# Performance work log

Measured on AMD Instinct MI355X. Metric: run time of the kernel, lower is better.

## Reference

```python
import jax, jax.numpy as jnp
import numpy as np

LN_EPS = 1e-5

def _layernorm(x, g, b):
    mu = jnp.mean(x, axis=-1, keepdims=True)
    var = jnp.mean(jnp.square(x - mu), axis=-1, keepdims=True)
    return (x - mu) * jax.lax.rsqrt(var + LN_EPS) * g + b

def setup_inputs() -> dict:
    key = jax.random.key(0)
    B, T, C = 8, 2048, 1024
    ks = jax.random.split(key, 16)
    s = 1.0 / np.sqrt(C)
    inp = {
        'x':   jax.random.normal(ks[0], (B, T, C), dtype=jnp.float32),
        'Wq':  jax.random.uniform(ks[1], (C, C), jnp.float32, -s, s),
        'bq':  jax.random.uniform(ks[2], (C,), jnp.float32, -s, s),
        'Wk':  jax.random.uniform(ks[3], (C, C), jnp.float32, -s, s),
        'bk':  jax.random.uniform(ks[4], (C,), jnp.float32, -s, s),
        'Wv':  jax.random.uniform(ks[5], (C, C), jnp.float32, -s, s),
        'bv':  jax.random.uniform(ks[6], (C,), jnp.float32, -s, s),
        'g1':  jnp.ones((C,), jnp.float32),
        'be1': jnp.zeros((C,), jnp.float32),
        'W1':  jax.random.uniform(ks[7], (C, C), jnp.float32, -s, s),
        'bf1': jax.random.uniform(ks[8], (C,), jnp.float32, -s, s),
        'W2':  jax.random.uniform(ks[9], (C, C), jnp.float32, -s, s),
        'bf2': jax.random.uniform(ks[10], (C,), jnp.float32, -s, s),
        'g2':  jnp.ones((C,), jnp.float32),
        'be2': jnp.zeros((C,), jnp.float32),
    }
    return inp

def reference(x, Wq, bq, Wk, bk, Wv, bv, g1, be1, W1, bf1, W2, bf2, g2, be2):
    B, T, C = x.shape
    q = x @ Wq + bq
    k = x @ Wk + bk
    v = x @ Wv + bv
    # FFT cross-correlation along time axis
    fq = jnp.fft.rfft(q, axis=1)
    fk = jnp.fft.rfft(k, axis=1)
    corr = jnp.fft.irfft(fq * jnp.conj(fk), n=T, axis=1)  # [B,T,C]
    weights = jax.nn.softmax(corr, axis=1)
    # einsum 'btd,btv->btd': weights * sum over v's channel dim
    attn = weights * jnp.sum(v, axis=-1, keepdims=True)
    x = _layernorm(x + attn, g1, be1)
    h = jax.nn.relu(x @ W1 + bf1) @ W2 + bf2
    x = _layernorm(x + h, g2, be2)
    return x
```

## Files before the change

kernel.cpp:

```cpp
#include <hip/hip_runtime.h>
#include <math.h>

#define B_DIM 8
#define T_DIM 2048
#define C_DIM 1024
#define BT_DIM (B_DIM * T_DIM)
#define FSZ ((size_t)BT_DIM * C_DIM)
#define LN_EPS 1e-5f

typedef __bf16 bf16x8 __attribute__((ext_vector_type(8)));
typedef _Float16 f16x8 __attribute__((ext_vector_type(8)));
typedef float f32x4 __attribute__((ext_vector_type(4)));

__device__ __forceinline__ unsigned short f2bf(float f) {
  __bf16 h = (__bf16)f;
  return __builtin_bit_cast(unsigned short, h);
}
__device__ __forceinline__ unsigned short f2h(float f) {
  _Float16 h = (_Float16)f;
  return __builtin_bit_cast(unsigned short, h);
}

__device__ __forceinline__ void gld16(const void* g, void* l) {
  __builtin_amdgcn_global_load_lds(
      (const __attribute__((address_space(1))) unsigned int*)g,
      (__attribute__((address_space(3))) unsigned int*)l, 16, 0, 0);
}

__device__ __forceinline__ int swz(int a) {
  return a ^ (((a >> 4) ^ (a >> 8)) & 15);
}

__device__ __forceinline__ int enc11(int f) {
  return ((f & 3) << 9) | (((f >> 2) & 3) << 7) | (((f >> 4) & 3) << 5) |
         (((f >> 6) & 3) << 3) | (((f >> 8) & 3) << 1) | ((f >> 10) & 1);
}

__global__ __launch_bounds__(256)
void cvt_split_f16_kernel(const float* __restrict__ x, unsigned short* __restrict__ hi,
                          unsigned short* __restrict__ lo) {
  size_t idx = ((size_t)blockIdx.x * 256 + threadIdx.x) * 4;
  float4 v = *(const float4*)(x + idx);
  float f[4] = {v.x, v.y, v.z, v.w};
  unsigned short hv[4], lv[4];
#pragma unroll
  for (int i = 0; i < 4; i++) {
    _Float16 hb = (_Float16)f[i];
    hv[i] = __builtin_bit_cast(unsigned short, hb);
    lv[i] = f2h(f[i] - (float)hb);
  }
  *(ushort4*)(hi + idx) = make_ushort4(hv[0], hv[1], hv[2], hv[3]);
  *(ushort4*)(lo + idx) = make_ushort4(lv[0], lv[1], lv[2], lv[3]);
}

__global__ __launch_bounds__(256)
void wtrans_f16_kernel(const float* __restrict__ W, unsigned short* __restrict__ Wt,
                       int K, int N) {
  __shared__ float tile[32][33];
  const int tid = threadIdx.x;
  const int tx = tid & 31, ty = tid >> 5;
  const int n0 = blockIdx.x * 32, k0 = blockIdx.y * 32;
#pragma unroll
  for (int i = 0; i < 4; i++) {
    int row = ty + i * 8;
    tile[row][tx] = W[(size_t)(k0 + row) * N + n0 + tx];
  }
  __syncthreads();
#pragma unroll
  for (int i = 0; i < 4; i++) {
    int row = ty + i * 8;
    Wt[(size_t)(n0 + row) * K + k0 + tx] = f2h(tile[tx][row]);
  }
}

__global__ __launch_bounds__(256)
void wtrans_kernel(const float* __restrict__ W, unsigned short* __restrict__ Wt,
                   int K, int N) {
  __shared__ float tile[32][33];
  const int tid = threadIdx.x;
  const int tx = tid & 31, ty = tid >> 5;
  const int n0 = blockIdx.x * 32, k0 = blockIdx.y * 32;
#pragma unroll
  for (int i = 0; i < 4; i++) {
    int row = ty + i * 8;
    tile[row][tx] = W[(size_t)(k0 + row) * N + n0 + tx];
  }
  __syncthreads();
#pragma unroll
  for (int i = 0; i < 4; i++) {
    int row = ty + i * 8;
    Wt[(size_t)(n0 + row) * K + k0 + tx] = f2bf(tile[tx][row]);
  }
}

__global__ __launch_bounds__(256)
void wv_rowsum_kernel(const float* __restrict__ Wv, const float* __restrict__ bv,
                      float* __restrict__ wvsum, float* __restrict__ bvsum) {
  const int r = blockIdx.x;
  const int tid = threadIdx.x;
  const float* src = (r < C_DIM) ? (Wv + (size_t)r * C_DIM) : bv;
  float4 t4 = *(const float4*)(src + (tid << 2));
  float s = t4.x + t4.y + t4.z + t4.w;
#pragma unroll
  for (int off = 32; off > 0; off >>= 1) s += __shfl_down(s, off);
  __shared__ float ps[4];
  if ((tid & 63) == 0) ps[tid >> 6] = s;
  __syncthreads();
  if (tid == 0) {
    float v = ps[0] + ps[1] + ps[2] + ps[3];
    if (r < C_DIM) wvsum[r] = v; else bvsum[0] = v;
  }
}

__global__ __launch_bounds__(256)
void sv_dot_kernel(const float* __restrict__ x, const float* __restrict__ wvsum,
                   const float* __restrict__ bvsum, float* __restrict__ sv) {
  const int r = blockIdx.x;
  const int tid = threadIdx.x;
  float4 a = *(const float4*)(x + (size_t)r * C_DIM + (tid << 2));
  float4 w = *(const float4*)(wvsum + (tid << 2));
  float s = a.x * w.x + a.y * w.y + a.z * w.z + a.w * w.w;
#pragma unroll
  for (int off = 32; off > 0; off >>= 1) s += __shfl_down(s, off);
  __shared__ float ps[4];
  if ((tid & 63) == 0) ps[tid >> 6] = s;
  __syncthreads();
  if (tid == 0) sv[r] = ps[0] + ps[1] + ps[2] + ps[3] + bvsum[0];
}

__global__ __launch_bounds__(256, 2)
void gemm_bf16_kernel(const __bf16* __restrict__ A, const __bf16* __restrict__ Bt,
                      const float* __restrict__ bias, float* Yf, unsigned short* Yb,
                      int K, int N, int do_relu) {
  __shared__ __align__(16) __bf16 As[128 * 32];
  __shared__ __align__(16) __bf16 Bs[128 * 32];
  const int tid = threadIdx.x;
  const int wave = tid >> 6, lane = tid & 63;
  const int wr = wave >> 1, wc = wave & 1;
  const int r15 = lane & 15, kq = lane >> 4;
  const int m0 = blockIdx.y * 128, n0 = blockIdx.x * 128;

  f32x4 acc[4][4] = {};

  for (int k0 = 0; k0 < K; k0 += 32) {
#pragma unroll
    for (int r = 0; r < 2; ++r) {
      int idx = r * 256 + tid;
      int row = idx >> 2;
      int ko = (idx & 3) ^ ((row >> 1) & 3);
      gld16(A + (size_t)(m0 + row) * K + k0 + ko * 8, &As[idx * 8]);
      gld16(Bt + (size_t)(n0 + row) * K + k0 + ko * 8, &Bs[idx * 8]);
    }
    __syncthreads();
    bf16x8 afr[4], bfr[4];
#pragma unroll
    for (int i = 0; i < 4; i++) {
      int ar = wr * 64 + i * 16 + r15;
      afr[i] = *(const bf16x8*)&As[(ar * 4 + (kq ^ ((ar >> 1) & 3))) * 8];
      int br = wc * 64 + i * 16 + r15;
      bfr[i] = *(const bf16x8*)&Bs[(br * 4 + (kq ^ ((br >> 1) & 3))) * 8];
    }
#pragma unroll
    for (int mi = 0; mi < 4; mi++)
#pragma unroll
      for (int ni = 0; ni < 4; ni++)
        acc[mi][ni] = __builtin_amdgcn_mfma_f32_16x16x32_bf16(afr[mi], bfr[ni], acc[mi][ni], 0, 0, 0);
    __syncthreads();
  }

  float bv[4];
#pragma unroll
  for (int ni = 0; ni < 4; ni++) bv[ni] = bias[n0 + wc * 64 + ni * 16 + r15];

#pragma unroll
  for (int mi = 0; mi < 4; mi++)
#pragma unroll
    for (int ni = 0; ni < 4; ni++) {
      const int n = n0 + wc * 64 + ni * 16 + r15;
#pragma unroll
      for (int r = 0; r < 4; r++) {
        const int m = m0 + wr * 64 + mi * 16 + kq * 4 + r;
        float v = acc[mi][ni][r] + bv[ni];
        if (do_relu) v = fmaxf(v, 0.f);
        if (Yf) Yf[(size_t)m * N + n] = v;
        if (Yb) Yb[(size_t)m * N + n] = f2bf(v);
      }
    }
}

__global__ __launch_bounds__(256, 2)
void gemm_qkT_f16_kernel(const _Float16* __restrict__ Ahi, const _Float16* __restrict__ Alo,
                         const _Float16* __restrict__ Bq, const _Float16* __restrict__ Bk,
                         const float* __restrict__ biasq, const float* __restrict__ biask,
                         float* __restrict__ Yq, float* __restrict__ Yk, int K, int N) {
  __shared__ __align__(16) _Float16 Ash[128 * 32];
  __shared__ __align__(16) _Float16 Asl[128 * 32];
  __shared__ __align__(16) _Float16 Bsq[128 * 32];
  __shared__ __align__(16) _Float16 Bsk[128 * 32];
  const int tid = threadIdx.x;
  const int wave = tid >> 6, lane = tid & 63;
  const int wr = wave >> 1, wc = wave & 1;
  const int r15 = lane & 15, kq = lane >> 4;
  const int m0 = blockIdx.y * 128, n0 = blockIdx.x * 128;

  f32x4 accq[4][4] = {};
  f32x4 acck[4][4] = {};

  for (int k0 = 0; k0 < K; k0 += 32) {
#pragma unroll
    for (int r = 0; r < 2; ++r) {
      int idx = r * 256 + tid;
      int row = idx >> 2;
      int ko = (idx & 3) ^ ((row >> 1) & 3);
      size_t ga = (size_t)(m0 + row) * K + k0 + ko * 8;
      size_t gb = (size_t)(n0 + row) * K + k0 + ko * 8;
      gld16(Ahi + ga, &Ash[idx * 8]);
      gld16(Alo + ga, &Asl[idx * 8]);
      gld16(Bq + gb, &Bsq[idx * 8]);
      gld16(Bk + gb, &Bsk[idx * 8]);
    }
    __syncthreads();
    f16x8 ah[4], al[4], bqf[4], bkf[4];
#pragma unroll
    for (int i = 0; i < 4; i++) {
      int ar = wr * 64 + i * 16 + r15;
      int as = (ar * 4 + (kq ^ ((ar >> 1) & 3))) * 8;
      ah[i] = *(const f16x8*)&Ash[as];
      al[i] = *(const f16x8*)&Asl[as];
      int br = wc * 64 + i * 16 + r15;
      int bs = (br * 4 + (kq ^ ((br >> 1) & 3))) * 8;
      bqf[i] = *(const f16x8*)&Bsq[bs];
      bkf[i] = *(const f16x8*)&Bsk[bs];
    }
#pragma unroll
    for (int mi = 0; mi < 4; mi++)
#pragma unroll
      for (int ni = 0; ni < 4; ni++) {
        f32x4 cq = accq[mi][ni];
        cq = __builtin_amdgcn_mfma_f32_16x16x32_f16(ah[mi], bqf[ni], cq, 0, 0, 0);
        cq = __builtin_amdgcn_mfma_f32_16x16x32_f16(al[mi], bqf[ni], cq, 0, 0, 0);
        accq[mi][ni] = cq;
        f32x4 ck = acck[mi][ni];
        ck = __builtin_amdgcn_mfma_f32_16x16x32_f16(ah[mi], bkf[ni], ck, 0, 0, 0);
        ck = __builtin_amdgcn_mfma_f32_16x16x32_f16(al[mi], bkf[ni], ck, 0, 0, 0);
        acck[mi][ni] = ck;
      }
    __syncthreads();
  }

  float bvq[4], bvk[4];
#pragma unroll
  for (int ni = 0; ni < 4; ni++) {
    bvq[ni] = biasq[n0 + wc * 64 + ni * 16 + r15];
    bvk[ni] = biask[n0 + wc * 64 + ni * 16 + r15];
  }

#pragma unroll
  for (int mi = 0; mi < 4; mi++) {
    const int mbase = m0 + wr * 64 + mi * 16 + kq * 4;
    const int bb = mbase >> 11;
    const int t = mbase & (T_DIM - 1);
#pragma unroll
    for (int ni = 0; ni < 4; ni++) {
      const int n = n0 + wc * 64 + ni * 16 + r15;
      const size_t o = ((size_t)bb * C_DIM + n) * T_DIM + t;
      *(float4*)(Yq + o) = make_float4(accq[mi][ni][0] + bvq[ni], accq[mi][ni][1] + bvq[ni],
                                       accq[mi][ni][2] + bvq[ni], accq[mi][ni][3] + bvq[ni]);
      *(float4*)(Yk + o) = make_float4(acck[mi][ni][0] + bvk[ni], acck[mi][ni][1] + bvk[ni],
                                       acck[mi][ni][2] + bvk[ni], acck[mi][ni][3] + bvk[ni]);
    }
  }
}

__device__ void fft_dif(float2* X, const float2* tw, int tid, float sgn) {
#pragma unroll
  for (int s = 0; s < 5; s++) {
    const int m = 512 >> (2 * s);
    const int jstep = 512 / m;
#pragma unroll
    for (int ii = 0; ii < 2; ii++) {
      const int i = tid + ii * 256;
      const int q = i & (m - 1);
      const int a0 = ((i - q) << 2) + q;
      float2 x0 = X[swz(a0)];
      float2 x1 = X[swz(a0 + m)];
      float2 x2 = X[swz(a0 + 2 * m)];
      float2 x3 = X[swz(a0 + 3 * m)];
      float2 t0 = make_float2(x0.x + x2.x, x0.y + x2.y);
      float2 t2 = make_float2(x0.x - x2.x, x0.y - x2.y);
      float2 t1 = make_float2(x1.x + x3.x, x1.y + x3.y);
      float2 t3 = make_float2(x1.x - x3.x, x1.y - x3.y);
      const float jx = -sgn * t3.y, jy = sgn * t3.x;
      float2 y0 = make_float2(t0.x + t1.x, t0.y + t1.y);
      float2 y1 = make_float2(t2.x + jx, t2.y + jy);
      float2 y2 = make_float2(t0.x - t1.x, t0.y - t1.y);
      float2 y3 = make_float2(t2.x - jx, t2.y - jy);
      const int j1 = q * jstep;
      float2 tv = tw[swz(j1)];
      const float c1 = tv.x, s1 = tv.y * sgn;
      const float c2 = c1 * c1 - s1 * s1, s2 = 2.f * c1 * s1;
      const float c3 = c2 * c1 - s2 * s1, s3 = c2 * s1 + s2 * c1;
      X[swz(a0)] = y0;
      X[swz(a0 + m)] = make_float2(c1 * y1.x - s1 * y1.y, c1 * y1.y + s1 * y1.x);
      X[swz(a0 + 2 * m)] = make_float2(c2 * y2.x - s2 * y2.y, c2 * y2.y + s2 * y2.x);
      X[swz(a0 + 3 * m)] = make_float2(c3 * y3.x - s3 * y3.y, c3 * y3.y + s3 * y3.x);
    }
    __syncthreads();
  }
#pragma unroll
  for (int ii = 0; ii < 4; ii++) {
    const int a = (tid + ii * 256) << 1;
    float2 u = X[swz(a)], v = X[swz(a + 1)];
    X[swz(a)] = make_float2(u.x + v.x, u.y + v.y);
    X[swz(a + 1)] = make_float2(u.x - v.x, u.y - v.y);
  }
  __syncthreads();
}

__device__ void fft_dit_inv(float2* X, const float2* tw, int tid) {
#pragma unroll
  for (int ii = 0; ii < 4; ii++) {
    const int a = (tid + ii * 256) << 1;
    float2 u = X[swz(a)], v = X[swz(a + 1)];
    X[swz(a)] = make_float2(u.x + v.x, u.y + v.y);
    X[swz(a + 1)] = make_float2(u.x - v.x, u.y - v.y);
  }
  __syncthreads();
#pragma unroll
  for (int s = 4; s >= 0; s--) {
    const int m = 512 >> (2 * s);
    const int jstep = 512 / m;
#pragma unroll
    for (int ii = 0; ii < 2; ii++) {
      const int i = tid + ii * 256;
      const int q = i & (m - 1);
      const int a0 = ((i - q) << 2) + q;
      float2 v0 = X[swz(a0)];
      float2 v1 = X[swz(a0 + m)];
      float2 v2 = X[swz(a0 + 2 * m)];
      float2 v3 = X[swz(a0 + 3 * m)];
      const int j1 = q * jstep;
      float2 tv = tw[swz(j1)];
      const float c1 = tv.x, s1 = tv.y;
      const float c2 = c1 * c1 - s1 * s1, s2 = 2.f * c1 * s1;
      const float c3 = c2 * c1 - s2 * s1, s3 = c2 * s1 + s2 * c1;
      float2 w1 = make_float2(c1 * v1.x - s1 * v1.y, c1 * v1.y + s1 * v1.x);
      float2 w2 = make_float2(c2 * v2.x - s2 * v2.y, c2 * v2.y + s2 * v2.x);
      float2 w3 = make_float2(c3 * v3.x - s3 * v3.y, c3 * v3.y + s3 * v3.x);
      float2 t0 = make_float2(v0.x + w2.x, v0.y + w2.y);
      float2 t2 = make_float2(v0.x - w2.x, v0.y - w2.y);
      float2 t1 = make_float2(w1.x + w3.x, w1.y + w3.y);
      float2 t3 = make_float2(w1.x - w3.x, w1.y - w3.y);
      const float jx = -t3.y, jy = t3.x;
      X[swz(a0)] = make_float2(t0.x + t1.x, t0.y + t1.y);
      X[swz(a0 + m)] = make_float2(t2.x + jx, t2.y + jy);
      X[swz(a0 + 2 * m)] = make_float2(t0.x - t1.x, t0.y - t1.y);
      X[swz(a0 + 3 * m)] = make_float2(t2.x - jx, t2.y - jy);
    }
    __syncthreads();
  }
}

__global__ __launch_bounds__(256)
void corr_fft_kernel(const float* qT, const float* kT, float* corrT,
                     float* __restrict__ Mv, float* __restrict__ Iv) {
  __shared__ float2 bA[2048];
  __shared__ float2 bB[2048];
  __shared__ float2 tw[512];
  __shared__ float2 red[4];
  const int tid = threadIdx.x;
  const int wave = tid >> 6, lane = tid & 63;
  const int b = blockIdx.y;
  const int c0 = blockIdx.x * 2;
  const float* q0 = qT + ((size_t)b * C_DIM + c0) * T_DIM;
  const float* k0p = kT + ((size_t)b * C_DIM + c0) * T_DIM;

#pragma unroll
  for (int jj = 0; jj < 2; jj++) {
    int j = tid + jj * 256;
    float sA, cA;
    __sincosf((float)j * (6.283185307179586f / 2048.0f), &sA, &cA);
    tw[swz(j)] = make_float2(cA, sA);
  }

#pragma unroll
  for (int jj = 0; jj < 8; jj++) {
    int t = tid + jj * 256;
    bA[swz(t)] = make_float2(q0[t], q0[t + T_DIM]);
    bB[swz(t)] = make_float2(k0p[t], k0p[t + T_DIM]);
  }
  __syncthreads();

  fft_dif(bA, tw, tid, -1.0f);
  fft_dif(bB, tw, tid, -1.0f);

#pragma unroll 1
  for (int f = tid; f <= 1024; f += 256) {
    const int g = (2048 - f) & 2047;
    const int p = swz(enc11(f));
    const int p2 = swz(enc11(g));
    float2 Zq = bA[p], Zq2 = bA[p2];
    float2 Zk = bB[p], Zk2 = bB[p2];
    float2 Aq = make_float2(0.5f * (Zq.x + Zq2.x), 0.5f * (Zq.y - Zq2.y));
    float2 Dq = make_float2(Zq.x - Zq2.x, Zq.y + Zq2.y);
    float2 Bq = make_float2(0.5f * Dq.y, -0.5f * Dq.x);
    float2 Ak = make_float2(0.5f * (Zk.x + Zk2.x), 0.5f * (Zk.y - Zk2.y));
    float2 Dk = make_float2(Zk.x - Zk2.x, Zk.y + Zk2.y);
    float2 Bk = make_float2(0.5f * Dk.y, -0.5f * Dk.x);
    float2 G = make_float2(Aq.x * Ak.x + Aq.y * Ak.y, Aq.y * Ak.x - Aq.x * Ak.y);
    float2 H = make_float2(Bq.x * Bk.x + Bq.y * Bk.y, Bq.y * Bk.x - Bq.x * Bk.y);
    bA[p] = make_float2(G.x - H.y, G.y + H.x);
    if (p2 != p) bA[p2] = make_float2(G.x + H.y, -G.y + H.x);
  }
  __syncthreads();

  fft_dit_inv(bA, tw, tid);

  float* o0 = corrT + ((size_t)b * C_DIM + c0) * T_DIM;
  const float sc = 1.0f / 2048.0f;
  float mx0 = -INFINITY, mx1 = -INFINITY;
#pragma unroll
  for (int jj = 0; jj < 8; jj++) {
    int t = tid + jj * 256;
    float2 o = bA[swz(t)];
    float v0 = o.x * sc, v1 = o.y * sc;
    o0[t] = v0;
    o0[t + T_DIM] = v1;
    mx0 = fmaxf(mx0, v0);
    mx1 = fmaxf(mx1, v1);
  }
#pragma unroll
  for (int off = 32; off > 0; off >>= 1) {
    mx0 = fmaxf(mx0, __shfl_down(mx0, off));
    mx1 = fmaxf(mx1, __shfl_down(mx1, off));
  }
  if (lane == 0) red[wave] = make_float2(mx0, mx1);
  __syncthreads();
  const float M0 = fmaxf(fmaxf(red[0].x, red[1].x), fmaxf(red[2].x, red[3].x));
  const float M1 = fmaxf(fmaxf(red[0].y, red[1].y), fmaxf(red[2].y, red[3].y));
  __syncthreads();
  float s0 = 0.f, s1 = 0.f;
#pragma unroll
  for (int jj = 0; jj < 8; jj++) {
    int t = tid + jj * 256;
    float2 o = bA[swz(t)];
    s0 += __expf(o.x * sc - M0);
    s1 += __expf(o.y * sc - M1);
  }
#pragma unroll
  for (int off = 32; off > 0; off >>= 1) {
    s0 += __shfl_down(s0, off);
    s1 += __shfl_down(s1, off);
  }
  if (lane == 0) red[wave] = make_float2(s0, s1);
  __syncthreads();
  if (tid == 0) {
    float S0 = red[0].x + red[1].x + red[2].x + red[3].x;
    float S1 = red[0].y + red[1].y + red[2].y + red[3].y;
    Mv[(size_t)b * C_DIM + c0] = M0;
    Mv[(size_t)b * C_DIM + c0 + 1] = M1;
    Iv[(size_t)b * C_DIM + c0] = 1.0f / S0;
    Iv[(size_t)b * C_DIM + c0 + 1] = 1.0f / S1;
  }
}

__global__ __launch_bounds__(256)
void attn_transpose_kernel(const float* __restrict__ corrT, const float* __restrict__ Mv,
                           const float* __restrict__ Iv, const float* __restrict__ sv,
                           float* __restrict__ attn) {
  __shared__ float tile[32][33];
  const int tid = threadIdx.x;
  const int tx = tid & 31, ty = tid >> 5;
  const int t0 = blockIdx.x * 32, c0 = blockIdx.y * 32, b = blockIdx.z;
  const float svv = sv[(size_t)b * T_DIM + t0 + tx];
#pragma unroll
  for (int i = 0; i < 4; i++) {
    const int c = c0 + ty + i * 8;
    const float M = Mv[(size_t)b * C_DIM + c];
    const float I = Iv[(size_t)b * C_DIM + c];
    float v = corrT[((size_t)b * C_DIM + c) * T_DIM + t0 + tx];
    tile[ty + i * 8][tx] = __expf(v - M) * I * svv;
  }
  __syncthreads();
#pragma unroll
  for (int i = 0; i < 4; i++) {
    const int t = t0 + ty + i * 8;
    attn[((size_t)b * T_DIM + t) * C_DIM + c0 + tx] = tile[tx][ty + i * 8];
  }
}

__global__ __launch_bounds__(256)
void add_ln_kernel(const float* __restrict__ A, const float* __restrict__ Bv,
                   const float* __restrict__ g, const float* __restrict__ be,
                   float* __restrict__ outf, unsigned short* outb) {
  const int r = blockIdx.x;
  const int tid = threadIdx.x;
  const size_t base = (size_t)r * C_DIM + (tid << 2);
  float4 a = *(const float4*)(A + base);
  float4 b = *(const float4*)(Bv + base);
  float x0 = a.x + b.x, x1 = a.y + b.y, x2 = a.z + b.z, x3 = a.w + b.w;
  float s = x0 + x1 + x2 + x3;
  float s2 = x0 * x0 + x1 * x1 + x2 * x2 + x3 * x3;
#pragma unroll
  for (int off = 32; off > 0; off >>= 1) {
    s += __shfl_down(s, off);
    s2 += __shfl_down(s2, off);
  }
  __shared__ float ps[4], ps2[4];
  if ((tid & 63) == 0) { ps[tid >> 6] = s; ps2[tid >> 6] = s2; }
  __syncthreads();
  float S = ps[0] + ps[1] + ps[2] + ps[3];
  float S2 = ps2[0] + ps2[1] + ps2[2] + ps2[3];
  const float mu = S * (1.0f / C_DIM);
  const float var = S2 * (1.0f / C_DIM) - mu * mu;
  const float rs = rsqrtf(var + LN_EPS);
  float4 gv = *(const float4*)(g + (tid << 2));
  float4 bev = *(const float4*)(be + (tid << 2));
  float o0 = (x0 - mu) * rs * gv.x + bev.x;
  float o1 = (x1 - mu) * rs * gv.y + bev.y;
  float o2 = (x2 - mu) * rs * gv.z + bev.z;
  float o3 = (x3 - mu) * rs * gv.w + bev.w;
  *(float4*)(outf + base) = make_float4(o0, o1, o2, o3);
  if (outb) *(ushort4*)(outb + base) = make_ushort4(f2bf(o0), f2bf(o1), f2bf(o2), f2bf(o3));
}

extern "C" void kernel_launch(void* const* d_in, const int* in_sizes, int n_in,
                              void* d_out, int out_size, void* d_ws, size_t ws_size,
                              hipStream_t stream) {
  const float* x   = (const float*)d_in[0];
  const float* Wq  = (const float*)d_in[1];
  const float* bq  = (const float*)d_in[2];
  const float* Wk  = (const float*)d_in[3];
  const float* bk  = (const float*)d_in[4];
  const float* Wv  = (const float*)d_in[5];
  const float* bv  = (const float*)d_in[6];
  const float* g1  = (const float*)d_in[7];
  const float* be1 = (const float*)d_in[8];
  const float* W1  = (const float*)d_in[9];
  const float* bf1 = (const float*)d_in[10];
  const float* W2  = (const float*)d_in[11];
  const float* bf2 = (const float*)d_in[12];
  const float* g2  = (const float*)d_in[13];
  const float* be2 = (const float*)d_in[14];
  float* out = (float*)d_out;

  float* ws = (float*)d_ws;
  float* qbuf = ws;
  float* kbuf = ws + FSZ;
  unsigned short* xhi = (unsigned short*)(ws + 2 * FSZ);
  unsigned short* xlo = xhi + FSZ;
  unsigned short* wA = xlo + FSZ;
  unsigned short* wB = wA + (size_t)C_DIM * C_DIM;
  float* sv = (float*)(wB + (size_t)C_DIM * C_DIM);
  float* wvsum = sv + BT_DIM;
  float* bvsum = wvsum + C_DIM;
  float* Mv = bvsum + 1;
  float* Iv = Mv + (size_t)B_DIM * C_DIM;

  const dim3 blk(256);
  const dim3 ggrid(C_DIM / 128, BT_DIM / 128);
  const dim3 tgrid(C_DIM / 32, C_DIM / 32);

  cvt_split_f16_kernel<<<dim3(FSZ / 1024), blk, 0, stream>>>(x, xhi, xlo);

  wv_rowsum_kernel<<<dim3(C_DIM + 1), blk, 0, stream>>>(Wv, bv, wvsum, bvsum);
  sv_dot_kernel<<<dim3(BT_DIM), blk, 0, stream>>>(x, wvsum, bvsum, sv);

  wtrans_f16_kernel<<<tgrid, blk, 0, stream>>>(Wq, wA, C_DIM, C_DIM);
  wtrans_f16_kernel<<<tgrid, blk, 0, stream>>>(Wk, wB, C_DIM, C_DIM);
  gemm_qkT_f16_kernel<<<ggrid, blk, 0, stream>>>((const _Float16*)xhi, (const _Float16*)xlo,
                                                 (const _Float16*)wA, (const _Float16*)wB,
                                                 bq, bk, qbuf, kbuf, C_DIM, C_DIM);

  corr_fft_kernel<<<dim3(C_DIM / 2, B_DIM), blk, 0, stream>>>(qbuf, kbuf, qbuf, Mv, Iv);

  attn_transpose_kernel<<<dim3(T_DIM / 32, C_DIM / 32, B_DIM), blk, 0, stream>>>(
      qbuf, Mv, Iv, sv, kbuf);

  add_ln_kernel<<<dim3(BT_DIM), blk, 0, stream>>>(x, kbuf, g1, be1, qbuf, xhi);

  wtrans_kernel<<<tgrid, blk, 0, stream>>>(W1, wA, C_DIM, C_DIM);
  wtrans_kernel<<<tgrid, blk, 0, stream>>>(W2, wB, C_DIM, C_DIM);

  gemm_bf16_kernel<<<ggrid, blk, 0, stream>>>((const __bf16*)xhi, (const __bf16*)wA,
                                              bf1, nullptr, xlo, C_DIM, C_DIM, 1);
  gemm_bf16_kernel<<<ggrid, blk, 0, stream>>>((const __bf16*)xlo, (const __bf16*)wB,
                                              bf2, kbuf, nullptr, C_DIM, C_DIM, 0);

  add_ln_kernel<<<dim3(BT_DIM), blk, 0, stream>>>(qbuf, kbuf, g2, be2, out, nullptr);
}
```

Measured before the change: 598.7 us.

## Rewrite QK GEMM as 512-thread, 256x128-tile, triple-buffered pipelined kernel

Replaces the Q/K projection GEMM with a 512-thread kernel that computes 256x128 output tiles. It uses a three-stage LDS ring with asynchronous global-to-LDS loads issued two K-steps ahead, waiting on vmcnt instead of using full syncthreads. MFMA bursts run at raised wave priority and the global loads are interleaved across four sub-phases. The aim is to hide memory latency and improve reuse of A operands, at the cost of much larger LDS use (about 144 KB per block), which limits occupancy.

```diff
diff --git a/kernel.cpp b/kernel.cpp
--- a/kernel.cpp
+++ b/kernel.cpp
@@ -188,81 +188,135 @@
     }
 }
 
-__global__ __launch_bounds__(256, 2)
-void gemm_qkT_f16_kernel(const _Float16* __restrict__ Ahi, const _Float16* __restrict__ Alo,
-                         const _Float16* __restrict__ Bq, const _Float16* __restrict__ Bk,
-                         const float* __restrict__ biasq, const float* __restrict__ biask,
-                         float* __restrict__ Yq, float* __restrict__ Yk, int K, int N) {
-  __shared__ __align__(16) _Float16 Ash[128 * 32];
-  __shared__ __align__(16) _Float16 Asl[128 * 32];
-  __shared__ __align__(16) _Float16 Bsq[128 * 32];
-  __shared__ __align__(16) _Float16 Bsk[128 * 32];
+__global__ __launch_bounds__(512, 2)
+void gemm_qkT_f16_8ph_kernel(const _Float16* __restrict__ Ahi, const _Float16* __restrict__ Alo,
+                             const _Float16* __restrict__ Bq, const _Float16* __restrict__ Bk,
+                             const float* __restrict__ biasq, const float* __restrict__ biask,
+                             float* __restrict__ Yq, float* __restrict__ Yk, int K, int N) {
+  __shared__ __align__(16) _Float16 AhL[3][256 * 32];
+  __shared__ __align__(16) _Float16 AlL[3][256 * 32];
+  __shared__ __align__(16) _Float16 BqL[3][128 * 32];
+  __shared__ __align__(16) _Float16 BkL[3][128 * 32];
+
   const int tid = threadIdx.x;
   const int wave = tid >> 6, lane = tid & 63;
-  const int wr = wave >> 1, wc = wave & 1;
+  const int wr = wave >> 2, wc = wave & 3;
   const int r15 = lane & 15, kq = lane >> 4;
-  const int m0 = blockIdx.y * 128, n0 = blockIdx.x * 128;
-
-  f32x4 accq[4][4] = {};
-  f32x4 acck[4][4] = {};
-
-  for (int k0 = 0; k0 < K; k0 += 32) {
-#pragma unroll
-    for (int r = 0; r < 2; ++r) {
-      int idx = r * 256 + tid;
-      int row = idx >> 2;
-      int ko = (idx & 3) ^ ((row >> 1) & 3);
-      size_t ga = (size_t)(m0 + row) * K + k0 + ko * 8;
-      size_t gb = (size_t)(n0 + row) * K + k0 + ko * 8;
-      gld16(Ahi + ga, &Ash[idx * 8]);
-      gld16(Alo + ga, &Asl[idx * 8]);
-      gld16(Bq + gb, &Bsq[idx * 8]);
-      gld16(Bk + gb, &Bsk[idx * 8]);
-    }
-    __syncthreads();
-    f16x8 ah[4], al[4], bqf[4], bkf[4];
-#pragma unroll
-    for (int i = 0; i < 4; i++) {
-      int ar = wr * 64 + i * 16 + r15;
-      int as = (ar * 4 + (kq ^ ((ar >> 1) & 3))) * 8;
-      ah[i] = *(const f16x8*)&Ash[as];
-      al[i] = *(const f16x8*)&Asl[as];
-      int br = wc * 64 + i * 16 + r15;
-      int bs = (br * 4 + (kq ^ ((br >> 1) & 3))) * 8;
-      bqf[i] = *(const f16x8*)&Bsq[bs];
-      bkf[i] = *(const f16x8*)&Bsk[bs];
-    }
-#pragma unroll
-    for (int mi = 0; mi < 4; mi++)
-#pragma unroll
-      for (int ni = 0; ni < 4; ni++) {
-        f32x4 cq = accq[mi][ni];
-        cq = __builtin_amdgcn_mfma_f32_16x16x32_f16(ah[mi], bqf[ni], cq, 0, 0, 0);
-        cq = __builtin_amdgcn_mfma_f32_16x16x32_f16(al[mi], bqf[ni], cq, 0, 0, 0);
-        accq[mi][ni] = cq;
-        f32x4 ck = acck[mi][ni];
-        ck = __builtin_amdgcn_mfma_f32_16x16x32_f16(ah[mi], bkf[ni], ck, 0, 0, 0);
-        ck = __builtin_amdgcn_mfma_f32_16x16x32_f16(al[mi], bkf[ni], ck, 0, 0, 0);
-        acck[mi][ni] = ck;
+  const int m0 = blockIdx.y * 256, n0 = blockIdx.x * 128;
+  const int NT = K >> 5;
+
+  const int row_a0 = tid >> 2;
+  const int row_a1 = row_a0 + 128;
+  const int ch = tid & 3;
+  const int ko0 = ch ^ ((row_a0 >> 1) & 3);
+  const int ko1 = ch ^ ((row_a1 >> 1) & 3);
+  const _Float16* agh0 = Ahi + (size_t)(m0 + row_a0) * K + ko0 * 8;
+  const _Float16* agl0 = Alo + (size_t)(m0 + row_a0) * K + ko0 * 8;
+  const _Float16* agh1 = Ahi + (size_t)(m0 + row_a1) * K + ko1 * 8;
+  const _Float16* agl1 = Alo + (size_t)(m0 + row_a1) * K + ko1 * 8;
+  const _Float16* bgq  = Bq  + (size_t)(n0 + row_a0) * K + ko0 * 8;
+  const _Float16* bgk  = Bk  + (size_t)(n0 + row_a0) * K + ko0 * 8;
+
+  const int ksel = kq ^ ((r15 >> 1) & 3);
+  const int aoff = (wr * 128 + r15) * 32 + ksel * 8;
+  const int boff = (wc * 32 + r15) * 32 + ksel * 8;
+
+  f32x4 accq[8][2] = {};
+  f32x4 acck[8][2] = {};
+
+  gld16(agh0 + 0, &AhL[0][(size_t)tid * 8]);
+  gld16(agl0 + 0, &AlL[0][(size_t)tid * 8]);
+  gld16(agh1 + 0, &AhL[0][(size_t)(tid + 512) * 8]);
+  gld16(agl1 + 0, &AlL[0][(size_t)(tid + 512) * 8]);
+  gld16(bgq + 0, &BqL[0][(size_t)tid * 8]);
+  gld16(bgk + 0, &BkL[0][(size_t)tid * 8]);
+  gld16(agh0 + 32, &AhL[1][(size_t)tid * 8]);
+  gld16(agl0 + 32, &AlL[1][(size_t)tid * 8]);
+  gld16(agh1 + 32, &AhL[1][(size_t)(tid + 512) * 8]);
+  gld16(agl1 + 32, &AlL[1][(size_t)(tid + 512) * 8]);
+  gld16(bgq + 32, &BqL[1][(size_t)tid * 8]);
+  gld16(bgk + 32, &BkL[1][(size_t)tid * 8]);
+
+  int bR = 0;
+  int bS = 2;
+
+  for (int j = 0; j < NT; ++j) {
+    if (j < NT - 1) {
+      asm volatile("s_waitcnt vmcnt(6)" ::: "memory");
+    } else {
+      asm volatile("s_waitcnt vmcnt(0)" ::: "memory");
+    }
+    __builtin_amdgcn_s_barrier();
+    __builtin_amdgcn_sched_barrier(0);
+
+    const int kk = (j + 2) * 32;
+    const bool doStage = (j + 2 < NT);
+
+    f16x8 bqf[2], bkf[2];
+#pragma unroll
+    for (int ni = 0; ni < 2; ++ni) {
+      bqf[ni] = *(const f16x8*)&BqL[bR][boff + ni * 512];
+      bkf[ni] = *(const f16x8*)&BkL[bR][boff + ni * 512];
+    }
+
+#pragma unroll
+    for (int p = 0; p < 4; ++p) {
+      f16x8 ah0 = *(const f16x8*)&AhL[bR][aoff + (2 * p + 0) * 512];
+      f16x8 al0 = *(const f16x8*)&AlL[bR][aoff + (2 * p + 0) * 512];
+      f16x8 ah1 = *(const f16x8*)&AhL[bR][aoff + (2 * p + 1) * 512];
+      f16x8 al1 = *(const f16x8*)&AlL[bR][aoff + (2 * p + 1) * 512];
+      if (doStage) {
+        if (p == 0) {
+          gld16(agh0 + kk, &AhL[bS][(size_t)tid * 8]);
+          gld16(agl0 + kk, &AlL[bS][(size_t)tid * 8]);
+        }
+        if (p == 1) {
+          gld16(agh1 + kk, &AhL[bS][(size_t)(tid + 512) * 8]);
+          gld16(agl1 + kk, &AlL[bS][(size_t)(tid + 512) * 8]);
+        }
+        if (p == 2) gld16(bgq + kk, &BqL[bS][(size_t)tid * 8]);
+        if (p == 3) gld16(bgk + kk, &BkL[bS][(size_t)tid * 8]);
       }
-    __syncthreads();
-  }
-
-  float bvq[4], bvk[4];
-#pragma unroll
-  for (int ni = 0; ni < 4; ni++) {
-    bvq[ni] = biasq[n0 + wc * 64 + ni * 16 + r15];
-    bvk[ni] = biask[n0 + wc * 64 + ni * 16 + r15];
-  }
-
-#pragma unroll
-  for (int mi = 0; mi < 4; mi++) {
-    const int mbase = m0 + wr * 64 + mi * 16 + kq * 4;
+      __builtin_amdgcn_s_barrier();
+      asm volatile("s_waitcnt lgkmcnt(0)" ::: "memory");
+      __builtin_amdgcn_sched_barrier(0);
+      __builtin_amdgcn_s_setprio(1);
+#pragma unroll
+      for (int m2 = 0; m2 < 2; ++m2) {
+        const int mi = 2 * p + m2;
+        const f16x8 ahv = m2 ? ah1 : ah0;
+        const f16x8 alv = m2 ? al1 : al0;
+#pragma unroll
+        for (int ni = 0; ni < 2; ++ni) {
+          accq[mi][ni] = __builtin_amdgcn_mfma_f32_16x16x32_f16(ahv, bqf[ni], accq[mi][ni], 0, 0, 0);
+          accq[mi][ni] = __builtin_amdgcn_mfma_f32_16x16x32_f16(alv, bqf[ni], accq[mi][ni], 0, 0, 0);
+          acck[mi][ni] = __builtin_amdgcn_mfma_f32_16x16x32_f16(ahv, bkf[ni], acck[mi][ni], 0, 0, 0);
+          acck[mi][ni] = __builtin_amdgcn_mfma_f32_16x16x32_f16(alv, bkf[ni], acck[mi][ni], 0, 0, 0);
+        }
+      }
+      __builtin_amdgcn_s_setprio(0);
+      __builtin_amdgcn_sched_barrier(0);
+    }
+
+    bR = (bR + 1 == 3) ? 0 : bR + 1;
+    bS = (bS + 1 == 3) ? 0 : bS + 1;
+  }
+
+  float bvq[2], bvk[2];
+#pragma unroll
+  for (int ni = 0; ni < 2; ++ni) {
+    bvq[ni] = biasq[n0 + wc * 32 + ni * 16 + r15];
+    bvk[ni] = biask[n0 + wc * 32 + ni * 16 + r15];
+  }
+
+#pragma unroll
+  for (int mi = 0; mi < 8; ++mi) {
+    const int mbase = m0 + wr * 128 + mi * 16 + kq * 4;
     const int bb = mbase >> 11;
     const int t = mbase & (T_DIM - 1);
 #pragma unroll
-    for (int ni = 0; ni < 4; ni++) {
-      const int n = n0 + wc * 64 + ni * 16 + r15;
+    for (int ni = 0; ni < 2; ++ni) {
+      const int n = n0 + wc * 32 + ni * 16 + r15;
       const size_t o = ((size_t)bb * C_DIM + n) * T_DIM + t;
       *(float4*)(Yq + o) = make_float4(accq[mi][ni][0] + bvq[ni], accq[mi][ni][1] + bvq[ni],
                                        accq[mi][ni][2] + bvq[ni], accq[mi][ni][3] + bvq[ni]);
@@ -559,6 +613,7 @@
 
   const dim3 blk(256);
   const dim3 ggrid(C_DIM / 128, BT_DIM / 128);
+  const dim3 qkgrid(C_DIM / 128, BT_DIM / 256);
   const dim3 tgrid(C_DIM / 32, C_DIM / 32);
 
   cvt_split_f16_kernel<<<dim3(FSZ / 1024), blk, 0, stream>>>(x, xhi, xlo);
@@ -568,9 +623,10 @@
 
   wtrans_f16_kernel<<<tgrid, blk, 0, stream>>>(Wq, wA, C_DIM, C_DIM);
   wtrans_f16_kernel<<<tgrid, blk, 0, stream>>>(Wk, wB, C_DIM, C_DIM);
-  gemm_qkT_f16_kernel<<<ggrid, blk, 0, stream>>>((const _Float16*)xhi, (const _Float16*)xlo,
-                                                 (const _Float16*)wA, (const _Float16*)wB,
-                                                 bq, bk, qbuf, kbuf, C_DIM, C_DIM);
+  gemm_qkT_f16_8ph_kernel<<<qkgrid, dim3(512), 0, stream>>>(
+      (const _Float16*)xhi, (const _Float16*)xlo,
+      (const _Float16*)wA, (const _Float16*)wB,
+      bq, bk, qbuf, kbuf, C_DIM, C_DIM);
 
   corr_fft_kernel<<<dim3(C_DIM / 2, B_DIM), blk, 0, stream>>>(qbuf, kbuf, qbuf, Mv, Iv);
 
```

Result: faster. 581.7 us (-2.8%).
